# Kernel tuning notes

Hardware: AMD Instinct MI355X
Metric: run time of the kernel (lower is better)

Reference implementation:

```python
import jax, jax.numpy as jnp
import numpy as np

N = 100000   # nodes
E = 3200000  # directed edges (avg degree 32)
T = 2048     # total flattened orders across all moves
M = 256      # number of moves (segments)


def _gat(x, src, dst, Wl, bl, Wr, br, att, b):
    # GATv2Conv (heads=1, eval mode -> attention dropout off), with self loops
    xl = x @ Wl.T + bl              # [N,10]
    xr = x @ Wr.T + br              # [N,10]
    sl = jnp.arange(N)
    s = jnp.concatenate([src, sl])
    d = jnp.concatenate([dst, sl])
    e = jax.nn.leaky_relu(xl[s] + xr[d], 0.2) @ att    # [E+N]
    emax = jax.ops.segment_max(e, d, num_segments=N)
    ex = jnp.exp(e - emax[d])
    den = jax.ops.segment_sum(ex, d, num_segments=N)
    return jax.ops.segment_sum((ex / den[d])[:, None] * xl[s], d, num_segments=N) + b


def setup_inputs() -> dict:
    key = jax.random.key(0)
    ks = iter(jax.random.split(key, 64))
    rn = lambda shape, s=0.1: jax.random.normal(next(ks), shape, jnp.float32) * s
    inp = {}
    inp['x1'] = rn((N, 15), 1.0)
    inp['x2'] = rn((1, 4), 1.0)
    src = jax.random.randint(next(ks), (E,), 0, N, jnp.int32)
    off = jax.random.randint(next(ks), (E,), 1, N, jnp.int32)
    inp['edge_src'] = src
    inp['edge_dst'] = ((src + off) % N).astype(jnp.int32)
    inp['move_type'] = jax.random.randint(next(ks), (T,), 0, 2, jnp.int32)
    inp['m_src'] = jax.random.randint(next(ks), (T,), 0, N, jnp.int32)
    inp['m_dst'] = jax.random.randint(next(ks), (T,), 0, N, jnp.int32)
    inp['m_target'] = jax.random.randint(next(ks), (T,), 0, N, jnp.int32)
    inp['m_armies'] = jax.random.uniform(next(ks), (T,), jnp.float32) * 10.0
    inp['move_id'] = (jnp.arange(T, dtype=jnp.int32) // (T // M))  # sorted, all segments non-empty
    # GATv2 layer params (in dims 15, 25, 25 -> out 10)
    for i, din in [(1, 15), (2, 25), (3, 25)]:
        inp[f'Wl{i}'] = rn((10, din)); inp[f'bl{i}'] = rn((10,))
        inp[f'Wr{i}'] = rn((10, din)); inp[f'br{i}'] = rn((10,))
        inp[f'att{i}'] = rn((10,));   inp[f'bias{i}'] = rn((10,))
    inp['lin_W'] = rn((15, 29)); inp['lin_b'] = rn((15,))
    inp['lin2_W'] = rn((1, 15)); inp['lin2_b'] = rn((1,))
    inp['aaa_W'] = rn((20, 48)); inp['aaa_b'] = rn((20,))
    inp['ccc_W'] = rn((20, 23)); inp['ccc_b'] = rn((20,))
    inp['attl_W'] = rn((1, 20)); inp['attl_b'] = rn((1,))
    inp['pi_W'] = rn((1, 20));   inp['pi_b'] = rn((1,))
    return inp


def reference(x1, x2, edge_src, edge_dst, move_type, m_src, m_dst, m_target, m_armies, move_id,
              Wl1, bl1, Wr1, br1, att1, bias1,
              Wl2, bl2, Wr2, br2, att2, bias2,
              Wl3, bl3, Wr3, br3, att3, bias3,
              lin_W, lin_b, lin2_W, lin2_b, aaa_W, aaa_b, ccc_W, ccc_b,
              attl_W, attl_b, pi_W, pi_b):
    h = jax.nn.relu(_gat(x1, edge_src, edge_dst, Wl1, bl1, Wr1, br1, att1, bias1))
    h = jax.nn.relu(_gat(jnp.concatenate([h, x1], 1), edge_src, edge_dst, Wl2, bl2, Wr2, br2, att2, bias2))
    x = jax.nn.relu(_gat(jnp.concatenate([h, x1], 1), edge_src, edge_dst, Wl3, bl3, Wr3, br3, att3, bias3))

    # per-order features (both branches computed, selected by move_type)
    extra = (0.6 * m_armies - 0.7 * (x1[m_dst, 3] + x1[m_dst, 4]))[:, None]
    feat_a = jnp.concatenate([x[m_src], x[m_dst], x1[m_src, 3:], x1[m_dst, 1:], m_armies[:, None], extra], axis=1)  # [T,48]
    a_out = jax.nn.relu(feat_a @ aaa_W.T + aaa_b)
    feat_d = jnp.concatenate([x[m_target], x1[m_target, 3:], m_armies[:, None]], axis=1)  # [T,23]
    d_out = jax.nn.relu(feat_d @ ccc_W.T + ccc_b)
    hm = jnp.where((move_type == 0)[:, None], a_out, d_out)  # [T,20]

    al = (hm @ attl_W.T + attl_b)[:, 0]   # [T]
    pi = (hm @ pi_W.T + pi_b)[:, 0]       # [T]
    amax = jax.ops.segment_max(al, move_id, num_segments=M)
    ex = jnp.exp(al - amax[move_id])
    den = jax.ops.segment_sum(ex, move_id, num_segments=M)
    p = jax.ops.segment_sum(ex / den[move_id] * pi, move_id, num_segments=M)  # [M]
    logp = jax.nn.log_softmax(p)

    x2t = jnp.tile(x2, (N, 1))
    v = jax.nn.relu(jnp.concatenate([x, x1, x2t], 1) @ lin_W.T + lin_b)
    V = jnp.tanh(jnp.mean(v @ lin2_W.T + lin2_b))
    return (V, logp)
```

## Files before the change

### kernel.cpp

```cpp
#include <hip/hip_runtime.h>
#include <cmath>

#define NN 100000
#define NE 3200000
#define TT 2048
#define MM 256
#define STR 16
#define HSTR 16
#define BSZ 64
#define NB 1563
#define EPB 16384
#define NBLK 196
#define SCAP 3072
#define PCAP 4096
#define CMAX 12

__device__ __forceinline__ void atomicMaxF(float* addr, float v) {
    if (v >= 0.f) atomicMax((int*)addr, __float_as_int(v));
    else          atomicMin((unsigned int*)addr, __float_as_uint(v));
}

__device__ __forceinline__ unsigned short f2bf(float x) {
    unsigned u = __float_as_uint(x);
    u += 0x7FFFu + ((u >> 16) & 1u);
    return (unsigned short)(u >> 16);
}

__device__ __forceinline__ void unpack10(uint4 q, unsigned q2, float* a) {
    a[0] = __uint_as_float(q.x << 16);
    a[1] = __uint_as_float(q.x & 0xFFFF0000u);
    a[2] = __uint_as_float(q.y << 16);
    a[3] = __uint_as_float(q.y & 0xFFFF0000u);
    a[4] = __uint_as_float(q.z << 16);
    a[5] = __uint_as_float(q.z & 0xFFFF0000u);
    a[6] = __uint_as_float(q.w << 16);
    a[7] = __uint_as_float(q.w & 0xFFFF0000u);
    a[8] = __uint_as_float(q2 << 16);
    a[9] = __uint_as_float(q2 & 0xFFFF0000u);
}

__global__ __launch_bounds__(256) void init_prep1_kernel(
    const float* __restrict__ x1,
    const float* __restrict__ Wl, const float* __restrict__ bl,
    const float* __restrict__ Wr, const float* __restrict__ br,
    unsigned short* __restrict__ xlh, unsigned short* __restrict__ xrh,
    int* __restrict__ pcursor, float* __restrict__ amax, float* __restrict__ Vsum)
{
    __shared__ float sWl[150], sWr[150], sbl[10], sbr[10];
    int tid = threadIdx.x;
    for (int i = tid; i < 150; i += 256) { sWl[i] = Wl[i]; sWr[i] = Wr[i]; }
    if (tid < 10) { sbl[tid] = bl[tid]; sbr[tid] = br[tid]; }
    __syncthreads();
    int gid = blockIdx.x * 256 + tid;
    if (gid < NB) pcursor[gid] = gid * PCAP;
    if (gid < MM) amax[gid] = -INFINITY;
    if (gid == 0) Vsum[0] = 0.f;
    int n = gid;
    if (n >= NN) return;

    float in[15];
    #pragma unroll
    for (int k = 0; k < 15; k++) in[k] = x1[n * 15 + k];

    unsigned* lp = (unsigned*)(xlh + n * HSTR);
    unsigned* rp = (unsigned*)(xrh + n * HSTR);
    #pragma unroll
    for (int jp = 0; jp < 5; jp++) {
        float sl0 = sbl[2 * jp], sr0 = sbr[2 * jp];
        float sl1 = sbl[2 * jp + 1], sr1 = sbr[2 * jp + 1];
        for (int k = 0; k < 15; k++) {
            float v = in[k];
            sl0 += v * sWl[(2 * jp) * 15 + k];
            sr0 += v * sWr[(2 * jp) * 15 + k];
            sl1 += v * sWl[(2 * jp + 1) * 15 + k];
            sr1 += v * sWr[(2 * jp + 1) * 15 + k];
        }
        lp[jp] = (unsigned)f2bf(sl0) | ((unsigned)f2bf(sl1) << 16);
        rp[jp] = (unsigned)f2bf(sr0) | ((unsigned)f2bf(sr1) << 16);
    }
}

__global__ __launch_bounds__(1024) void scatter_kernel(const int* __restrict__ src,
                                                       const int* __restrict__ dst,
                                                       int* __restrict__ pcursor,
                                                       int* __restrict__ srtp) {
    __shared__ int ent[EPB];
    __shared__ int cnt[NB];
    __shared__ int cur[NB];
    __shared__ int gbase[NB];
    __shared__ int psc[1024];
    int tid = threadIdx.x;
    for (int i = tid; i < NB; i += 1024) cnt[i] = 0;
    __syncthreads();
    int base = blockIdx.x * EPB;
    int end = base + EPB; if (end > NE) end = NE;
    for (int i = base + tid * 4; i < end; i += 4096) {
        int4 d4 = *(const int4*)(dst + i);
        atomicAdd(&cnt[d4.x >> 6], 1);
        atomicAdd(&cnt[d4.y >> 6], 1);
        atomicAdd(&cnt[d4.z >> 6], 1);
        atomicAdd(&cnt[d4.w >> 6], 1);
    }
    __syncthreads();
    const int PT = (NB + 1023) / 1024;
    int t0 = tid * PT;
    int s = 0;
    #pragma unroll
    for (int j = 0; j < PT; j++) { int idx = t0 + j; if (idx < NB) s += cnt[idx]; }
    psc[tid] = s;
    __syncthreads();
    for (int off = 1; off < 1024; off <<= 1) {
        int v = (tid >= off) ? psc[tid - off] : 0;
        __syncthreads();
        psc[tid] += v;
        __syncthreads();
    }
    int run = psc[tid] - s;
    #pragma unroll
    for (int j = 0; j < PT; j++) {
        int idx = t0 + j;
        if (idx < NB) { cur[idx] = run; run += cnt[idx]; }
    }
    for (int b = tid; b < NB; b += 1024) {
        int n = cnt[b];
        gbase[b] = n ? atomicAdd(&pcursor[b], (n + 15) & ~15) : 0;
    }
    __syncthreads();
    for (int i = base + tid * 4; i < end; i += 4096) {
        int4 d4 = *(const int4*)(dst + i);
        int4 s4 = *(const int4*)(src + i);
        int d, b, off;
        d = d4.x; b = d >> 6; off = atomicAdd(&cur[b], 1); ent[off] = ((d & 63) << 17) | s4.x;
        d = d4.y; b = d >> 6; off = atomicAdd(&cur[b], 1); ent[off] = ((d & 63) << 17) | s4.y;
        d = d4.z; b = d >> 6; off = atomicAdd(&cur[b], 1); ent[off] = ((d & 63) << 17) | s4.z;
        d = d4.w; b = d >> 6; off = atomicAdd(&cur[b], 1); ent[off] = ((d & 63) << 17) | s4.w;
    }
    __syncthreads();
    for (int b = tid; b < NB; b += 1024) {
        int n = cnt[b];
        if (!n) continue;
        int lb = cur[b] - n;
        int gb = gbase[b];
        int p16 = (n + 15) & ~15;
        for (int k = 0; k < p16; k += 4) {
            int4 v;
            v.x = (k + 0 < n) ? ent[lb + k + 0] : -1;
            v.y = (k + 1 < n) ? ent[lb + k + 1] : -1;
            v.z = (k + 2 < n) ? ent[lb + k + 2] : -1;
            v.w = (k + 3 < n) ? ent[lb + k + 3] : -1;
            *(int4*)(srtp + gb + k) = v;
        }
    }
}

__global__ __launch_bounds__(512) void sort2_kernel(int* __restrict__ srtp,
                                                    const int* __restrict__ pcursor,
                                                    int* __restrict__ bcounts) {
    __shared__ int ent[PCAP];
    __shared__ int ent2[SCAP];
    __shared__ int cnts[BSZ];
    __shared__ int curs[BSZ];
    int b = blockIdx.x, tid = threadIdx.x;
    int p0 = b * PCAP;
    int pcnt = pcursor[b] - p0;
    if (pcnt > PCAP) pcnt = PCAP;
    if (tid < BSZ) cnts[tid] = 0;
    __syncthreads();
    for (int i = tid; i < pcnt; i += 512) {
        int p = srtp[p0 + i];
        ent[i] = p;
        if (p >= 0) atomicAdd(&cnts[p >> 17], 1);
    }
    __syncthreads();
    if (tid == 0) {
        int run = 0;
        for (int k = 0; k < BSZ; k++) { curs[k] = run; run += cnts[k]; }
    }
    __syncthreads();
    for (int i = tid; i < pcnt; i += 512) {
        int p = ent[i];
        if (p >= 0) {
            int pos = atomicAdd(&curs[p >> 17], 1);
            ent2[pos] = p;
        }
    }
    __syncthreads();
    int cnt = curs[BSZ - 1];
    for (int i = tid; i < cnt; i += 512) srtp[p0 + i] = ent2[i];
    if (tid == 0) bcounts[b] = cnt;
}

__global__ __launch_bounds__(256, 4) void gather_mid_kernel(
    const int* __restrict__ srtp, const int* __restrict__ bcounts,
    const unsigned short* __restrict__ xlh, const unsigned short* __restrict__ xrh,
    const float* __restrict__ att, const float* __restrict__ bias,
    const float* __restrict__ x1,
    const float* __restrict__ Wl2, const float* __restrict__ bl2,
    const float* __restrict__ Wr2, const float* __restrict__ br2,
    unsigned short* __restrict__ xlh_out, unsigned short* __restrict__ xrh_out)
{
    __shared__ float accs[BSZ * 11];
    __shared__ float xrs[BSZ * 11];
    __shared__ float sat[10], sbias[10];
    __shared__ float sWl2[250], sWr2[250], sbl2[10], sbr2[10];
    __shared__ float inbuf[BSZ * 25];
    int b = blockIdx.x, tid = threadIdx.x;
    int n0 = b * BSZ;
    int nv = NN - n0; if (nv > BSZ) nv = BSZ;
    if (tid < 10) { sat[tid] = att[tid]; sbias[tid] = bias[tid];
                    sbl2[tid] = bl2[tid]; sbr2[tid] = br2[tid]; }
    for (int i = tid; i < 250; i += 256) { sWl2[i] = Wl2[i]; sWr2[i] = Wr2[i]; }
    for (int i = tid; i < nv * 15; i += 256)
        inbuf[(i / 15) * 25 + 10 + (i % 15)] = x1[n0 * 15 + i];
    __syncthreads();

    if (tid < BSZ) {
        int n = n0 + tid;
        if (n < NN) {
            const unsigned short* lr = xlh + n * HSTR;
            const unsigned short* rr = xrh + n * HSTR;
            uint4 ql = *(const uint4*)lr;  unsigned ql2 = *(const unsigned*)(lr + 8);
            uint4 qr = *(const uint4*)rr;  unsigned qr2 = *(const unsigned*)(rr + 8);
            float a[10], r[10];
            unpack10(ql, ql2, a);
            unpack10(qr, qr2, r);
            #pragma unroll
            for (int k = 0; k < 10; k++) xrs[tid * 11 + k] = r[k];
            float e = 0.f;
            #pragma unroll
            for (int k = 0; k < 10; k++) {
                float t = a[k] + r[k];
                t = t > 0.f ? t : 0.2f * t;
                e += sat[k] * t;
            }
            float ex = __expf(e);
            #pragma unroll
            for (int k = 0; k < 10; k++) accs[tid * 11 + k] = ex * a[k];
            accs[tid * 11 + 10] = ex;
        } else {
            #pragma unroll
            for (int k = 0; k < 11; k++) { accs[tid * 11 + k] = 0.f; xrs[tid * 11 + k] = 0.f; }
        }
    }
    __syncthreads();

    int i0 = b * PCAP;
    int cnt = bcounts[b];
    int C = (cnt + 255) >> 8;
    int a0 = i0 + tid * C;
    int a1 = a0 + C; if (a1 > i0 + cnt) a1 = i0 + cnt;
    int len = a1 - a0; if (len < 0) len = 0;
    if (len > 0) {
        int ps[CMAX];
        #pragma unroll
        for (int i = 0; i < CMAX; i++) ps[i] = (i < len) ? srtp[a0 + i] : -1;

        const unsigned short* row0 = xlh + (ps[0] & 0x1FFFF) * HSTR;
        uint4 q = *(const uint4*)row0;
        unsigned q2 = *(const unsigned*)(row0 + 8);
        int cur = ps[0] >> 17;
        float racc[10];
        #pragma unroll
        for (int k = 0; k < 10; k++) racc[k] = 0.f;
        float rden = 0.f;
        #pragma unroll
        for (int i = 0; i < CMAX; i++) {
            if (i >= len) break;
            uint4 qn = q; unsigned q2n = q2;
            if (i + 1 < len) {
                const unsigned short* rn = xlh + (ps[i + 1] & 0x1FFFF) * HSTR;
                qn = *(const uint4*)rn;
                q2n = *(const unsigned*)(rn + 8);
            }
            int ld = ps[i] >> 17;
            if (ld != cur) {
                float* ac = accs + cur * 11;
                #pragma unroll
                for (int k = 0; k < 10; k++) atomicAdd(ac + k, racc[k]);
                atomicAdd(ac + 10, rden);
                #pragma unroll
                for (int k = 0; k < 10; k++) racc[k] = 0.f;
                rden = 0.f;
                cur = ld;
            }
            float a[10];
            unpack10(q, q2, a);
            const float* r = xrs + ld * 11;
            float e = 0.f;
            #pragma unroll
            for (int k = 0; k < 10; k++) {
                float t = a[k] + r[k];
                t = t > 0.f ? t : 0.2f * t;
                e += sat[k] * t;
            }
            float ex = __expf(e);
            rden += ex;
            #pragma unroll
            for (int k = 0; k < 10; k++) racc[k] += ex * a[k];
            q = qn; q2 = q2n;
        }
        float* ac = accs + cur * 11;
        #pragma unroll
        for (int k = 0; k < 10; k++) atomicAdd(ac + k, racc[k]);
        atomicAdd(ac + 10, rden);
    }
    __syncthreads();

    if (tid < nv) {
        float inv = 1.f / accs[tid * 11 + 10];
        #pragma unroll
        for (int k = 0; k < 10; k++) {
            float v = accs[tid * 11 + k] * inv + sbias[k];
            inbuf[tid * 25 + k] = v > 0.f ? v : 0.f;
        }
    }
    __syncthreads();

    for (int w = tid; w < BSZ * 10; w += 256) {
        int node = w / 10, word = w % 10;
        if (node >= nv) continue;
        const float* in = inbuf + node * 25;
        int jp = word % 5;
        const float* Wb = (word < 5) ? sWl2 : sWr2;
        const float* bb = (word < 5) ? sbl2 : sbr2;
        float s0 = bb[2 * jp], s1 = bb[2 * jp + 1];
        for (int k = 0; k < 25; k++) {
            float v = in[k];
            s0 += v * Wb[(2 * jp) * 25 + k];
            s1 += v * Wb[(2 * jp + 1) * 25 + k];
        }
        unsigned short* outp = ((word < 5) ? xlh_out : xrh_out) + (n0 + node) * HSTR;
        ((unsigned*)outp)[jp] = (unsigned)f2bf(s0) | ((unsigned)f2bf(s1) << 16);
    }
}

__global__ __launch_bounds__(256, 4) void gather_last_kernel(
    const int* __restrict__ srtp, const int* __restrict__ bcounts,
    const unsigned short* __restrict__ xlh, const unsigned short* __restrict__ xrh,
    const float* __restrict__ att, const float* __restrict__ bias,
    const float* __restrict__ x1, const float* __restrict__ x2,
    const float* __restrict__ lin_W, const float* __restrict__ lin_b,
    const float* __restrict__ lin2_W, const float* __restrict__ lin2_b,
    float* __restrict__ hout, float* __restrict__ Vsum)
{
    __shared__ float accs[BSZ * 11];
    __shared__ float xrs[BSZ * 11];
    __shared__ float sat[10], sbias[10];
    __shared__ float sLW[15 * 29], sLb[15], sW2[15];
    __shared__ float inbuf[BSZ * 29];
    __shared__ float bsum;
    __shared__ float slin2b;
    int b = blockIdx.x, tid = threadIdx.x;
    int n0 = b * BSZ;
    int nv = NN - n0; if (nv > BSZ) nv = BSZ;
    if (tid < 10) { sat[tid] = att[tid]; sbias[tid] = bias[tid]; }
    for (int i = tid; i < 15 * 29; i += 256) sLW[i] = lin_W[i];
    if (tid < 15) { sLb[tid] = lin_b[tid]; sW2[tid] = lin2_W[tid]; }
    if (tid == 0) { slin2b = lin2_b[0]; bsum = 0.f; }
    for (int i = tid; i < nv * 15; i += 256)
        inbuf[(i / 15) * 29 + 10 + (i % 15)] = x1[n0 * 15 + i];
    if (tid < 4 * BSZ && (tid >> 2) < nv) inbuf[(tid >> 2) * 29 + 25 + (tid & 3)] = x2[tid & 3];
    __syncthreads();

    if (tid < BSZ) {
        int n = n0 + tid;
        if (n < NN) {
            const unsigned short* lr = xlh + n * HSTR;
            const unsigned short* rr = xrh + n * HSTR;
            uint4 ql = *(const uint4*)lr;  unsigned ql2 = *(const unsigned*)(lr + 8);
            uint4 qr = *(const uint4*)rr;  unsigned qr2 = *(const unsigned*)(rr + 8);
            float a[10], r[10];
            unpack10(ql, ql2, a);
            unpack10(qr, qr2, r);
            #pragma unroll
            for (int k = 0; k < 10; k++) xrs[tid * 11 + k] = r[k];
            float e = 0.f;
            #pragma unroll
            for (int k = 0; k < 10; k++) {
                float t = a[k] + r[k];
                t = t > 0.f ? t : 0.2f * t;
                e += sat[k] * t;
            }
            float ex = __expf(e);
            #pragma unroll
            for (int k = 0; k < 10; k++) accs[tid * 11 + k] = ex * a[k];
            accs[tid * 11 + 10] = ex;
        } else {
            #pragma unroll
            for (int k = 0; k < 11; k++) { accs[tid * 11 + k] = 0.f; xrs[tid * 11 + k] = 0.f; }
        }
    }
    __syncthreads();

    int i0 = b * PCAP;
    int cnt = bcounts[b];
    int C = (cnt + 255) >> 8;
    int a0 = i0 + tid * C;
    int a1 = a0 + C; if (a1 > i0 + cnt) a1 = i0 + cnt;
    int len = a1 - a0; if (len < 0) len = 0;
    if (len > 0) {
        int ps[CMAX];
        #pragma unroll
        for (int i = 0; i < CMAX; i++) ps[i] = (i < len) ? srtp[a0 + i] : -1;

        const unsigned short* row0 = xlh + (ps[0] & 0x1FFFF) * HSTR;
        uint4 q = *(const uint4*)row0;
        unsigned q2 = *(const unsigned*)(row0 + 8);
        int cur = ps[0] >> 17;
        float racc[10];
        #pragma unroll
        for (int k = 0; k < 10; k++) racc[k] = 0.f;
        float rden = 0.f;
        #pragma unroll
        for (int i = 0; i < CMAX; i++) {
            if (i >= len) break;
            uint4 qn = q; unsigned q2n = q2;
            if (i + 1 < len) {
                const unsigned short* rn = xlh + (ps[i + 1] & 0x1FFFF) * HSTR;
                qn = *(const uint4*)rn;
                q2n = *(const unsigned*)(rn + 8);
            }
            int ld = ps[i] >> 17;
            if (ld != cur) {
                float* ac = accs + cur * 11;
                #pragma unroll
                for (int k = 0; k < 10; k++) atomicAdd(ac + k, racc[k]);
                atomicAdd(ac + 10, rden);
                #pragma unroll
                for (int k = 0; k < 10; k++) racc[k] = 0.f;
                rden = 0.f;
                cur = ld;
            }
            float a[10];
            unpack10(q, q2, a);
            const float* r = xrs + ld * 11;
            float e = 0.f;
            #pragma unroll
            for (int k = 0; k < 10; k++) {
                float t = a[k] + r[k];
                t = t > 0.f ? t : 0.2f * t;
                e += sat[k] * t;
            }
            float ex = __expf(e);
            rden += ex;
            #pragma unroll
            for (int k = 0; k < 10; k++) racc[k] += ex * a[k];
            q = qn; q2 = q2n;
        }
        float* ac = accs + cur * 11;
        #pragma unroll
        for (int k = 0; k < 10; k++) atomicAdd(ac + k, racc[k]);
        atomicAdd(ac + 10, rden);
    }
    __syncthreads();

    if (tid < nv) {
        float inv = 1.f / accs[tid * 11 + 10];
        #pragma unroll
        for (int k = 0; k < 10; k++) {
            float v = accs[tid * 11 + k] * inv + sbias[k];
            inbuf[tid * 29 + k] = v > 0.f ? v : 0.f;
        }
    }
    __syncthreads();

    for (int w = tid; w < BSZ * 10; w += 256) {
        int node = w / 10, k = w % 10;
        if (node < nv) hout[(n0 + node) * STR + k] = inbuf[node * 29 + k];
    }
    for (int w = tid; w < BSZ * 15; w += 256) {
        int node = w / 15, j = w % 15;
        if (node >= nv) continue;
        const float* in = inbuf + node * 29;
        float s = sLb[j];
        for (int k = 0; k < 29; k++) s += in[k] * sLW[j * 29 + k];
        if (s > 0.f) atomicAdd(&bsum, s * sW2[j]);
    }
    __syncthreads();
    if (tid == 0) atomicAdd(Vsum, bsum + (float)nv * slin2b);
}

__global__ __launch_bounds__(256) void orders_kernel(
    const float* __restrict__ x, const float* __restrict__ x1,
    const int* __restrict__ move_type, const int* __restrict__ m_src,
    const int* __restrict__ m_dst, const int* __restrict__ m_target,
    const float* __restrict__ m_armies, const int* __restrict__ move_id,
    const float* __restrict__ aaa_W, const float* __restrict__ aaa_b,
    const float* __restrict__ ccc_W, const float* __restrict__ ccc_b,
    const float* __restrict__ attl_W, const float* __restrict__ attl_b,
    const float* __restrict__ pi_W, const float* __restrict__ pi_b,
    float* __restrict__ al_out, float* __restrict__ pi_out, float* __restrict__ amax)
{
    __shared__ float sA[20 * 48], sC[20 * 23], sAb[20], sCb[20];
    int tid = threadIdx.x;
    for (int i = tid; i < 20 * 48; i += 256) sA[i] = aaa_W[i];
    for (int i = tid; i < 20 * 23; i += 256) sC[i] = ccc_W[i];
    if (tid < 20) { sAb[tid] = aaa_b[tid]; sCb[tid] = ccc_b[tid]; }
    __syncthreads();
    int t = blockIdx.x * 256 + tid;
    if (t >= TT) return;

    float armies = m_armies[t];
    float hm[20];
    if (move_type[t] == 0) {
        int sn = m_src[t], dn = m_dst[t];
        float f[48];
        #pragma unroll
        for (int k = 0; k < 10; k++) f[k] = x[sn * STR + k];
        #pragma unroll
        for (int k = 0; k < 10; k++) f[10 + k] = x[dn * STR + k];
        #pragma unroll
        for (int k = 0; k < 12; k++) f[20 + k] = x1[sn * 15 + 3 + k];
        #pragma unroll
        for (int k = 0; k < 14; k++) f[32 + k] = x1[dn * 15 + 1 + k];
        f[46] = armies;
        f[47] = 0.6f * armies - 0.7f * (x1[dn * 15 + 3] + x1[dn * 15 + 4]);
        #pragma unroll
        for (int j = 0; j < 20; j++) {
            float s = sAb[j];
            for (int k = 0; k < 48; k++) s += f[k] * sA[j * 48 + k];
            hm[j] = s > 0.f ? s : 0.f;
        }
    } else {
        int tg = m_target[t];
        float f[23];
        #pragma unroll
        for (int k = 0; k < 10; k++) f[k] = x[tg * STR + k];
        #pragma unroll
        for (int k = 0; k < 12; k++) f[10 + k] = x1[tg * 15 + 3 + k];
        f[22] = armies;
        #pragma unroll
        for (int j = 0; j < 20; j++) {
            float s = sCb[j];
            for (int k = 0; k < 23; k++) s += f[k] * sC[j * 23 + k];
            hm[j] = s > 0.f ? s : 0.f;
        }
    }
    float a = attl_b[0], p = pi_b[0];
    #pragma unroll
    for (int j = 0; j < 20; j++) { a += hm[j] * attl_W[j]; p += hm[j] * pi_W[j]; }
    al_out[t] = a;
    pi_out[t] = p;
    atomicMaxF(&amax[move_id[t]], a);
}

__global__ __launch_bounds__(256) void final2_kernel(
    const float* __restrict__ al, const float* __restrict__ piv,
    const int* __restrict__ move_id, const float* __restrict__ amax,
    const float* __restrict__ Vsum, float* __restrict__ out)
{
    __shared__ float den_s[MM], num_s[MM];
    __shared__ float sh[256];
    __shared__ float s_max, s_sum;
    int m = threadIdx.x;
    den_s[m] = 0.f; num_s[m] = 0.f;
    __syncthreads();
    for (int t = m; t < TT; t += 256) {
        int mid = move_id[t];
        float ex = __expf(al[t] - amax[mid]);
        atomicAdd(&den_s[mid], ex);
        atomicAdd(&num_s[mid], ex * piv[t]);
    }
    __syncthreads();
    float p = num_s[m] / den_s[m];
    sh[m] = p;
    __syncthreads();
    for (int off = 128; off > 0; off >>= 1) {
        if (m < off) sh[m] = fmaxf(sh[m], sh[m + off]);
        __syncthreads();
    }
    if (m == 0) s_max = sh[0];
    __syncthreads();
    float e = __expf(p - s_max);
    sh[m] = e;
    __syncthreads();
    for (int off = 128; off > 0; off >>= 1) {
        if (m < off) sh[m] += sh[m + off];
        __syncthreads();
    }
    if (m == 0) s_sum = sh[0];
    __syncthreads();
    out[1 + m] = p - s_max - logf(s_sum);
    if (m == 0) out[0] = tanhf(Vsum[0] / (float)NN);
}

extern "C" void kernel_launch(void* const* d_in, const int* in_sizes, int n_in,
                              void* d_out, int out_size, void* d_ws, size_t ws_size,
                              hipStream_t stream) {
    const float* x1        = (const float*)d_in[0];
    const float* x2        = (const float*)d_in[1];
    const int*   esrc      = (const int*)d_in[2];
    const int*   edst      = (const int*)d_in[3];
    const int*   move_type = (const int*)d_in[4];
    const int*   m_src     = (const int*)d_in[5];
    const int*   m_dst     = (const int*)d_in[6];
    const int*   m_target  = (const int*)d_in[7];
    const float* m_armies  = (const float*)d_in[8];
    const int*   move_id   = (const int*)d_in[9];
    const float* W[3][6];
    for (int l = 0; l < 3; l++)
        for (int j = 0; j < 6; j++)
            W[l][j] = (const float*)d_in[10 + l * 6 + j];
    const float* lin_W  = (const float*)d_in[28];
    const float* lin_b  = (const float*)d_in[29];
    const float* lin2_W = (const float*)d_in[30];
    const float* lin2_b = (const float*)d_in[31];
    const float* aaa_W  = (const float*)d_in[32];
    const float* aaa_b  = (const float*)d_in[33];
    const float* ccc_W  = (const float*)d_in[34];
    const float* ccc_b  = (const float*)d_in[35];
    const float* attl_W = (const float*)d_in[36];
    const float* attl_b = (const float*)d_in[37];
    const float* pi_W   = (const float*)d_in[38];
    const float* pi_b   = (const float*)d_in[39];

    float* ws = (float*)d_ws;
    float* hA    = ws; ws += NN * STR;
    float* al    = ws; ws += TT;
    float* piv   = ws; ws += TT;
    float* amax  = ws; ws += MM;
    float* Vsum  = ws; ws += 1;
    unsigned short* xlhA = (unsigned short*)ws; ws += NN * HSTR / 2;
    unsigned short* xrhA = (unsigned short*)ws; ws += NN * HSTR / 2;
    unsigned short* xlhB = (unsigned short*)ws; ws += NN * HSTR / 2;
    unsigned short* xrhB = (unsigned short*)ws; ws += NN * HSTR / 2;
    int* iws = (int*)ws;
    int* pcursor = iws; iws += NB;
    int* bcounts = iws; iws += NB;
    int* srtp    = iws; iws += NB * PCAP;

    dim3 blk(256);
    dim3 gN((NN + 255) / 256);
    dim3 gT(TT / 256);

    init_prep1_kernel<<<gN, blk, 0, stream>>>(x1, W[0][0], W[0][1], W[0][2], W[0][3],
                                              xlhA, xrhA, pcursor, amax, Vsum);
    scatter_kernel<<<dim3(NBLK), dim3(1024), 0, stream>>>(esrc, edst, pcursor, srtp);
    sort2_kernel<<<dim3(NB), dim3(512), 0, stream>>>(srtp, pcursor, bcounts);

    gather_mid_kernel<<<dim3(NB), blk, 0, stream>>>(srtp, bcounts, xlhA, xrhA,
                                                    W[0][4], W[0][5], x1,
                                                    W[1][0], W[1][1], W[1][2], W[1][3],
                                                    xlhB, xrhB);
    gather_mid_kernel<<<dim3(NB), blk, 0, stream>>>(srtp, bcounts, xlhB, xrhB,
                                                    W[1][4], W[1][5], x1,
                                                    W[2][0], W[2][1], W[2][2], W[2][3],
                                                    xlhA, xrhA);
    gather_last_kernel<<<dim3(NB), blk, 0, stream>>>(srtp, bcounts, xlhA, xrhA,
                                                     W[2][4], W[2][5], x1, x2,
                                                     lin_W, lin_b, lin2_W, lin2_b,
                                                     hA, Vsum);

    orders_kernel<<<gT, blk, 0, stream>>>(hA, x1, move_type, m_src, m_dst, m_target,
                                          m_armies, move_id, aaa_W, aaa_b, ccc_W, ccc_b,
                                          attl_W, attl_b, pi_W, pi_b, al, piv, amax);
    final2_kernel<<<dim3(1), blk, 0, stream>>>(al, piv, move_id, amax, Vsum, (float*)d_out);
}
```

Measured before the change: 402.2 us.

## Fuse bucket sort into first GAT gather layer and deepen row prefetch

Merges the per-block second-level sort kernel into the first GAT gather kernel, so layer one reads its sorted edge list straight from shared memory. This drops one launch and one global round trip of the sorted list. The edge gather loop now prefetches two rows ahead instead of one, to hide more gather latency. The cost is more shared memory and registers in the fused kernel, and a smaller thread count (256 instead of 512) for the sort phase.

```diff
diff --git a/kernel.cpp b/kernel.cpp
--- a/kernel.cpp
+++ b/kernel.cpp
@@ -39,6 +39,95 @@
     a[9] = __uint_as_float(q2 & 0xFFFF0000u);
 }
 
+#define GATHER_MAIN_LOOP(LEN, PS_EXPR)                                              \
+    if ((LEN) > 0) {                                                                \
+        int ps[CMAX];                                                               \
+        _Pragma("unroll")                                                           \
+        for (int i = 0; i < CMAX; i++) ps[i] = (i < (LEN)) ? (PS_EXPR) : -1;        \
+        const unsigned short* row;                                                  \
+        row = xlh + (ps[0] & 0x1FFFF) * HSTR;                                       \
+        uint4 qa = *(const uint4*)row;  unsigned q2a = *(const unsigned*)(row + 8); \
+        uint4 qb = qa; unsigned q2b = q2a;                                          \
+        if ((LEN) > 1) {                                                            \
+            row = xlh + (ps[1] & 0x1FFFF) * HSTR;                                   \
+            qb = *(const uint4*)row;  q2b = *(const unsigned*)(row + 8);            \
+        }                                                                           \
+        int cur = ps[0] >> 17;                                                      \
+        float racc[10];                                                             \
+        _Pragma("unroll")                                                           \
+        for (int k = 0; k < 10; k++) racc[k] = 0.f;                                 \
+        float rden = 0.f;                                                           \
+        _Pragma("unroll")                                                           \
+        for (int i = 0; i < CMAX; i++) {                                            \
+            if (i >= (LEN)) break;                                                  \
+            uint4 qc = qb; unsigned q2c = q2b;                                      \
+            if (i + 2 < (LEN)) {                                                    \
+                row = xlh + (ps[i + 2] & 0x1FFFF) * HSTR;                           \
+                qc = *(const uint4*)row;  q2c = *(const unsigned*)(row + 8);        \
+            }                                                                       \
+            int ld = ps[i] >> 17;                                                   \
+            if (ld != cur) {                                                        \
+                float* ac = accs + cur * 11;                                        \
+                _Pragma("unroll")                                                   \
+                for (int k = 0; k < 10; k++) atomicAdd(ac + k, racc[k]);            \
+                atomicAdd(ac + 10, rden);                                           \
+                _Pragma("unroll")                                                   \
+                for (int k = 0; k < 10; k++) racc[k] = 0.f;                         \
+                rden = 0.f;                                                         \
+                cur = ld;                                                           \
+            }                                                                       \
+            float a[10];                                                            \
+            unpack10(qa, q2a, a);                                                   \
+            const float* r = xrs + ld * 11;                                         \
+            float e = 0.f;                                                          \
+            _Pragma("unroll")                                                       \
+            for (int k = 0; k < 10; k++) {                                          \
+                float t = a[k] + r[k];                                              \
+                t = t > 0.f ? t : 0.2f * t;                                         \
+                e += sat[k] * t;                                                    \
+            }                                                                       \
+            float ex = __expf(e);                                                   \
+            rden += ex;                                                             \
+            _Pragma("unroll")                                                       \
+            for (int k = 0; k < 10; k++) racc[k] += ex * a[k];                      \
+            qa = qb; q2a = q2b; qb = qc; q2b = q2c;                                 \
+        }                                                                           \
+        float* ac = accs + cur * 11;                                                \
+        _Pragma("unroll")                                                           \
+        for (int k = 0; k < 10; k++) atomicAdd(ac + k, racc[k]);                    \
+        atomicAdd(ac + 10, rden);                                                   \
+    }
+
+#define SELF_ROW_INIT                                                               \
+    if (tid < BSZ) {                                                                \
+        int n = n0 + tid;                                                           \
+        if (n < NN) {                                                               \
+            const unsigned short* lr = xlh + n * HSTR;                              \
+            const unsigned short* rr = xrh + n * HSTR;                              \
+            uint4 ql = *(const uint4*)lr;  unsigned ql2 = *(const unsigned*)(lr + 8); \
+            uint4 qr = *(const uint4*)rr;  unsigned qr2 = *(const unsigned*)(rr + 8); \
+            float a[10], r[10];                                                     \
+            unpack10(ql, ql2, a);                                                   \
+            unpack10(qr, qr2, r);                                                   \
+            _Pragma("unroll")                                                       \
+            for (int k = 0; k < 10; k++) xrs[tid * 11 + k] = r[k];                  \
+            float e = 0.f;                                                          \
+            _Pragma("unroll")                                                       \
+            for (int k = 0; k < 10; k++) {                                          \
+                float t = a[k] + r[k];                                              \
+                t = t > 0.f ? t : 0.2f * t;                                         \
+                e += sat[k] * t;                                                    \
+            }                                                                       \
+            float ex = __expf(e);                                                   \
+            _Pragma("unroll")                                                       \
+            for (int k = 0; k < 10; k++) accs[tid * 11 + k] = ex * a[k];            \
+            accs[tid * 11 + 10] = ex;                                               \
+        } else {                                                                    \
+            _Pragma("unroll")                                                       \
+            for (int k = 0; k < 11; k++) { accs[tid * 11 + k] = 0.f; xrs[tid * 11 + k] = 0.f; } \
+        }                                                                           \
+    }
+
 __global__ __launch_bounds__(256) void init_prep1_kernel(
     const float* __restrict__ x1,
     const float* __restrict__ Wl, const float* __restrict__ bl,
@@ -153,31 +242,51 @@
     }
 }
 
-__global__ __launch_bounds__(512) void sort2_kernel(int* __restrict__ srtp,
-                                                    const int* __restrict__ pcursor,
-                                                    int* __restrict__ bcounts) {
+__global__ __launch_bounds__(256) void gather_first_kernel(
+    int* __restrict__ srtp, const int* __restrict__ pcursor, int* __restrict__ bcounts,
+    const unsigned short* __restrict__ xlh, const unsigned short* __restrict__ xrh,
+    const float* __restrict__ att, const float* __restrict__ bias,
+    const float* __restrict__ x1,
+    const float* __restrict__ Wl2, const float* __restrict__ bl2,
+    const float* __restrict__ Wr2, const float* __restrict__ br2,
+    unsigned short* __restrict__ xlh_out, unsigned short* __restrict__ xrh_out)
+{
     __shared__ int ent[PCAP];
     __shared__ int ent2[SCAP];
     __shared__ int cnts[BSZ];
     __shared__ int curs[BSZ];
+    __shared__ float accs[BSZ * 11];
+    __shared__ float xrs[BSZ * 11];
+    __shared__ float sat[10], sbias[10];
+    __shared__ float sWl2[250], sWr2[250], sbl2[10], sbr2[10];
+    __shared__ float inbuf[BSZ * 25];
     int b = blockIdx.x, tid = threadIdx.x;
+    int n0 = b * BSZ;
+    int nv = NN - n0; if (nv > BSZ) nv = BSZ;
+    if (tid < 10) { sat[tid] = att[tid]; sbias[tid] = bias[tid];
+                    sbl2[tid] = bl2[tid]; sbr2[tid] = br2[tid]; }
+    for (int i = tid; i < 250; i += 256) { sWl2[i] = Wl2[i]; sWr2[i] = Wr2[i]; }
+    for (int i = tid; i < nv * 15; i += 256)
+        inbuf[(i / 15) * 25 + 10 + (i % 15)] = x1[n0 * 15 + i];
+    if (tid < BSZ) cnts[tid] = 0;
+    __syncthreads();
+
     int p0 = b * PCAP;
     int pcnt = pcursor[b] - p0;
     if (pcnt > PCAP) pcnt = PCAP;
-    if (tid < BSZ) cnts[tid] = 0;
-    __syncthreads();
-    for (int i = tid; i < pcnt; i += 512) {
+    for (int i = tid; i < pcnt; i += 256) {
         int p = srtp[p0 + i];
         ent[i] = p;
         if (p >= 0) atomicAdd(&cnts[p >> 17], 1);
     }
+    SELF_ROW_INIT
     __syncthreads();
     if (tid == 0) {
         int run = 0;
         for (int k = 0; k < BSZ; k++) { curs[k] = run; run += cnts[k]; }
     }
     __syncthreads();
-    for (int i = tid; i < pcnt; i += 512) {
+    for (int i = tid; i < pcnt; i += 256) {
         int p = ent[i];
         if (p >= 0) {
             int pos = atomicAdd(&curs[p >> 17], 1);
@@ -186,8 +295,42 @@
     }
     __syncthreads();
     int cnt = curs[BSZ - 1];
-    for (int i = tid; i < cnt; i += 512) srtp[p0 + i] = ent2[i];
+    for (int i = tid; i < cnt; i += 256) srtp[p0 + i] = ent2[i];
     if (tid == 0) bcounts[b] = cnt;
+
+    int C = (cnt + 255) >> 8;
+    int l0 = tid * C;
+    int l1 = l0 + C; if (l1 > cnt) l1 = cnt;
+    int len = l1 - l0; if (len < 0) len = 0;
+    GATHER_MAIN_LOOP(len, ent2[l0 + i])
+    __syncthreads();
+
+    if (tid < nv) {
+        float inv = 1.f / accs[tid * 11 + 10];
+        #pragma unroll
+        for (int k = 0; k < 10; k++) {
+            float v = accs[tid * 11 + k] * inv + sbias[k];
+            inbuf[tid * 25 + k] = v > 0.f ? v : 0.f;
+        }
+    }
+    __syncthreads();
+
+    for (int w = tid; w < BSZ * 10; w += 256) {
+        int node = w / 10, word = w % 10;
+        if (node >= nv) continue;
+        const float* in = inbuf + node * 25;
+        int jp = word % 5;
+        const float* Wb = (word < 5) ? sWl2 : sWr2;
+        const float* bb = (word < 5) ? sbl2 : sbr2;
+        float s0 = bb[2 * jp], s1 = bb[2 * jp + 1];
+        for (int k = 0; k < 25; k++) {
+            float v = in[k];
+            s0 += v * Wb[(2 * jp) * 25 + k];
+            s1 += v * Wb[(2 * jp + 1) * 25 + k];
+        }
+        unsigned short* outp = ((word < 5) ? xlh_out : xrh_out) + (n0 + node) * HSTR;
+        ((unsigned*)outp)[jp] = (unsigned)f2bf(s0) | ((unsigned)f2bf(s1) << 16);
+    }
 }
 
 __global__ __launch_bounds__(256, 4) void gather_mid_kernel(
@@ -212,36 +355,7 @@
     for (int i = tid; i < 250; i += 256) { sWl2[i] = Wl2[i]; sWr2[i] = Wr2[i]; }
     for (int i = tid; i < nv * 15; i += 256)
         inbuf[(i / 15) * 25 + 10 + (i % 15)] = x1[n0 * 15 + i];
-    __syncthreads();
-
-    if (tid < BSZ) {
-        int n = n0 + tid;
-        if (n < NN) {
-            const unsigned short* lr = xlh + n * HSTR;
-            const unsigned short* rr = xrh + n * HSTR;
-            uint4 ql = *(const uint4*)lr;  unsigned ql2 = *(const unsigned*)(lr + 8);
-            uint4 qr = *(const uint4*)rr;  unsigned qr2 = *(const unsigned*)(rr + 8);
-            float a[10], r[10];
-            unpack10(ql, ql2, a);
-            unpack10(qr, qr2, r);
-            #pragma unroll
-            for (int k = 0; k < 10; k++) xrs[tid * 11 + k] = r[k];
-            float e = 0.f;
-            #pragma unroll
-            for (int k = 0; k < 10; k++) {
-                float t = a[k] + r[k];
-                t = t > 0.f ? t : 0.2f * t;
-                e += sat[k] * t;
-            }
-            float ex = __expf(e);
-            #pragma unroll
-            for (int k = 0; k < 10; k++) accs[tid * 11 + k] = ex * a[k];
-            accs[tid * 11 + 10] = ex;
-        } else {
-            #pragma unroll
-            for (int k = 0; k < 11; k++) { accs[tid * 11 + k] = 0.f; xrs[tid * 11 + k] = 0.f; }
-        }
-    }
+    SELF_ROW_INIT
     __syncthreads();
 
     int i0 = b * PCAP;
@@ -250,60 +364,7 @@
     int a0 = i0 + tid * C;
     int a1 = a0 + C; if (a1 > i0 + cnt) a1 = i0 + cnt;
     int len = a1 - a0; if (len < 0) len = 0;
-    if (len > 0) {
-        int ps[CMAX];
-        #pragma unroll
-        for (int i = 0; i < CMAX; i++) ps[i] = (i < len) ? srtp[a0 + i] : -1;
-
-        const unsigned short* row0 = xlh + (ps[0] & 0x1FFFF) * HSTR;
-        uint4 q = *(const uint4*)row0;
-        unsigned q2 = *(const unsigned*)(row0 + 8);
-        int cur = ps[0] >> 17;
-        float racc[10];
-        #pragma unroll
-        for (int k = 0; k < 10; k++) racc[k] = 0.f;
-        float rden = 0.f;
-        #pragma unroll
-        for (int i = 0; i < CMAX; i++) {
-            if (i >= len) break;
-            uint4 qn = q; unsigned q2n = q2;
-            if (i + 1 < len) {
-                const unsigned short* rn = xlh + (ps[i + 1] & 0x1FFFF) * HSTR;
-                qn = *(const uint4*)rn;
-                q2n = *(const unsigned*)(rn + 8);
-            }
-            int ld = ps[i] >> 17;
-            if (ld != cur) {
-                float* ac = accs + cur * 11;
-                #pragma unroll
-                for (int k = 0; k < 10; k++) atomicAdd(ac + k, racc[k]);
-                atomicAdd(ac + 10, rden);
-                #pragma unroll
-                for (int k = 0; k < 10; k++) racc[k] = 0.f;
-                rden = 0.f;
-                cur = ld;
-            }
-            float a[10];
-            unpack10(q, q2, a);
-            const float* r = xrs + ld * 11;
-            float e = 0.f;
-            #pragma unroll
-            for (int k = 0; k < 10; k++) {
-                float t = a[k] + r[k];
-                t = t > 0.f ? t : 0.2f * t;
-                e += sat[k] * t;
-            }
-            float ex = __expf(e);
-            rden += ex;
-            #pragma unroll
-            for (int k = 0; k < 10; k++) racc[k] += ex * a[k];
-            q = qn; q2 = q2n;
-        }
-        float* ac = accs + cur * 11;
-        #pragma unroll
-        for (int k = 0; k < 10; k++) atomicAdd(ac + k, racc[k]);
-        atomicAdd(ac + 10, rden);
-    }
+    GATHER_MAIN_LOOP(len, srtp[a0 + i])
     __syncthreads();
 
     if (tid < nv) {
@@ -360,36 +421,7 @@
     for (int i = tid; i < nv * 15; i += 256)
         inbuf[(i / 15) * 29 + 10 + (i % 15)] = x1[n0 * 15 + i];
     if (tid < 4 * BSZ && (tid >> 2) < nv) inbuf[(tid >> 2) * 29 + 25 + (tid & 3)] = x2[tid & 3];
-    __syncthreads();
-
-    if (tid < BSZ) {
-        int n = n0 + tid;
-        if (n < NN) {
-            const unsigned short* lr = xlh + n * HSTR;
-            const unsigned short* rr = xrh + n * HSTR;
-            uint4 ql = *(const uint4*)lr;  unsigned ql2 = *(const unsigned*)(lr + 8);
-            uint4 qr = *(const uint4*)rr;  unsigned qr2 = *(const unsigned*)(rr + 8);
-            float a[10], r[10];
-            unpack10(ql, ql2, a);
-            unpack10(qr, qr2, r);
-            #pragma unroll
-            for (int k = 0; k < 10; k++) xrs[tid * 11 + k] = r[k];
-            float e = 0.f;
-            #pragma unroll
-            for (int k = 0; k < 10; k++) {
-                float t = a[k] + r[k];
-                t = t > 0.f ? t : 0.2f * t;
-                e += sat[k] * t;
-            }
-            float ex = __expf(e);
-            #pragma unroll
-            for (int k = 0; k < 10; k++) accs[tid * 11 + k] = ex * a[k];
-            accs[tid * 11 + 10] = ex;
-        } else {
-            #pragma unroll
-            for (int k = 0; k < 11; k++) { accs[tid * 11 + k] = 0.f; xrs[tid * 11 + k] = 0.f; }
-        }
-    }
+    SELF_ROW_INIT
     __syncthreads();
 
     int i0 = b * PCAP;
@@ -398,60 +430,7 @@
     int a0 = i0 + tid * C;
     int a1 = a0 + C; if (a1 > i0 + cnt) a1 = i0 + cnt;
     int len = a1 - a0; if (len < 0) len = 0;
-    if (len > 0) {
-        int ps[CMAX];
-        #pragma unroll
-        for (int i = 0; i < CMAX; i++) ps[i] = (i < len) ? srtp[a0 + i] : -1;
-
-        const unsigned short* row0 = xlh + (ps[0] & 0x1FFFF) * HSTR;
-        uint4 q = *(const uint4*)row0;
-        unsigned q2 = *(const unsigned*)(row0 + 8);
-        int cur = ps[0] >> 17;
-        float racc[10];
-        #pragma unroll
-        for (int k = 0; k < 10; k++) racc[k] = 0.f;
-        float rden = 0.f;
-        #pragma unroll
-        for (int i = 0; i < CMAX; i++) {
-            if (i >= len) break;
-            uint4 qn = q; unsigned q2n = q2;
-            if (i + 1 < len) {
-                const unsigned short* rn = xlh + (ps[i + 1] & 0x1FFFF) * HSTR;
-                qn = *(const uint4*)rn;
-                q2n = *(const unsigned*)(rn + 8);
-            }
-            int ld = ps[i] >> 17;
-            if (ld != cur) {
-                float* ac = accs + cur * 11;
-                #pragma unroll
-                for (int k = 0; k < 10; k++) atomicAdd(ac + k, racc[k]);
-                atomicAdd(ac + 10, rden);
-                #pragma unroll
-                for (int k = 0; k < 10; k++) racc[k] = 0.f;
-                rden = 0.f;
-                cur = ld;
-            }
-            float a[10];
-            unpack10(q, q2, a);
-            const float* r = xrs + ld * 11;
-            float e = 0.f;
-            #pragma unroll
-            for (int k = 0; k < 10; k++) {
-                float t = a[k] + r[k];
-                t = t > 0.f ? t : 0.2f * t;
-                e += sat[k] * t;
-            }
-            float ex = __expf(e);
-            rden += ex;
-            #pragma unroll
-            for (int k = 0; k < 10; k++) racc[k] += ex * a[k];
-            q = qn; q2 = q2n;
-        }
-        float* ac = accs + cur * 11;
-        #pragma unroll
-        for (int k = 0; k < 10; k++) atomicAdd(ac + k, racc[k]);
-        atomicAdd(ac + 10, rden);
-    }
+    GATHER_MAIN_LOOP(len, srtp[a0 + i])
     __syncthreads();
 
     if (tid < nv) {
@@ -636,12 +615,11 @@
     init_prep1_kernel<<<gN, blk, 0, stream>>>(x1, W[0][0], W[0][1], W[0][2], W[0][3],
                                               xlhA, xrhA, pcursor, amax, Vsum);
     scatter_kernel<<<dim3(NBLK), dim3(1024), 0, stream>>>(esrc, edst, pcursor, srtp);
-    sort2_kernel<<<dim3(NB), dim3(512), 0, stream>>>(srtp, pcursor, bcounts);
-
-    gather_mid_kernel<<<dim3(NB), blk, 0, stream>>>(srtp, bcounts, xlhA, xrhA,
-                                                    W[0][4], W[0][5], x1,
-                                                    W[1][0], W[1][1], W[1][2], W[1][3],
-                                                    xlhB, xrhB);
+
+    gather_first_kernel<<<dim3(NB), blk, 0, stream>>>(srtp, pcursor, bcounts, xlhA, xrhA,
+                                                      W[0][4], W[0][5], x1,
+                                                      W[1][0], W[1][1], W[1][2], W[1][3],
+                                                      xlhB, xrhB);
     gather_mid_kernel<<<dim3(NB), blk, 0, stream>>>(srtp, bcounts, xlhB, xrhB,
                                                     W[1][4], W[1][5], x1,
                                                     W[2][0], W[2][1], W[2][2], W[2][3],
```

Result: slower. 414.5 us (+3.1%).
